# Kernel optimization log

Measured on AMD Instinct MI355X. Metric: run time of the kernel, lower is better.

The kernel has to match this reference:

```python
import jax, jax.numpy as jnp
import numpy as np
from jax import lax

EPS = 1e-5  # BatchNorm eps (torch default)


def _bn_relu_conv3x3_s2(x, bn_w, bn_b, bn_m, bn_v, w, b):
    # eval-mode BatchNorm2d -> ReLU -> conv3x3 stride 2 pad 1 (NCHW)
    inv = bn_w / jnp.sqrt(bn_v + EPS)
    y = x * inv[None, :, None, None] + (bn_b - bn_m * inv)[None, :, None, None]
    y = jax.nn.relu(y)
    y = lax.conv_general_dilated(y, w, window_strides=(2, 2),
                                 padding=((1, 1), (1, 1)),
                                 dimension_numbers=("NCHW", "OIHW", "NCHW"))
    return y + b[None, :, None, None]


def _avgpool2x2(x):
    B, C, H, W = x.shape
    return x.reshape(B, C, H // 2, 2, W // 2, 2).mean(axis=(3, 5))


def setup_inputs() -> dict:
    key = jax.random.key(0)
    ks = jax.random.split(key, 24)
    C, C3 = 128, 128 // 3
    d = {"x": jax.random.normal(ks[0], (8, C, 96, 96), jnp.float32)}
    for i, p in enumerate(["f", "g", "h"]):
        base = 1 + i * 6
        d[p + "_bn_w"] = jax.random.uniform(ks[base], (C,), jnp.float32, 0.5, 1.5)
        d[p + "_bn_b"] = jax.random.normal(ks[base + 1], (C,), jnp.float32) * 0.1
        d[p + "_bn_m"] = jax.random.normal(ks[base + 2], (C,), jnp.float32) * 0.1
        d[p + "_bn_v"] = jax.random.uniform(ks[base + 3], (C,), jnp.float32, 0.5, 1.5)
        d[p + "_w"] = jax.random.normal(ks[base + 4], (C, C, 3, 3), jnp.float32) * (1.0 / np.sqrt(9 * C))
        d[p + "_b"] = jax.random.normal(ks[base + 5], (C,), jnp.float32) * 0.01
    d["se_cw"] = jax.random.normal(ks[19], (C3, 2 * C), jnp.float32) * (1.0 / np.sqrt(2 * C))
    d["se_cb"] = jax.random.normal(ks[20], (C3,), jnp.float32) * 0.01
    d["se_uw"] = jax.random.normal(ks[21], (C, C3), jnp.float32) * (1.0 / np.sqrt(C3))
    d["se_ub"] = jax.random.normal(ks[22], (C,), jnp.float32) * 0.01
    d["gamma"] = jax.random.normal(ks[23], (1,), jnp.float32) * 0.5
    return d


def reference(x, f_bn_w, f_bn_b, f_bn_m, f_bn_v, f_w, f_b,
              g_bn_w, g_bn_b, g_bn_m, g_bn_v, g_w, g_b,
              h_bn_w, h_bn_b, h_bn_m, h_bn_v, h_w, h_b,
              se_cw, se_cb, se_uw, se_ub, gamma):
    B, C, H, W = x.shape
    left = _avgpool2x2(x)  # isPrimary=False branch -> [B,C,H/2,W/2]

    f = _bn_relu_conv3x3_s2(x, f_bn_w, f_bn_b, f_bn_m, f_bn_v, f_w, f_b)
    g = _bn_relu_conv3x3_s2(x, g_bn_w, g_bn_b, g_bn_m, g_bn_v, g_w, g_b)
    h = _bn_relu_conv3x3_s2(x, h_bn_w, h_bn_b, h_bn_m, h_bn_v, h_w, h_b)

    Ho, Wo = f.shape[2], f.shape[3]
    N = Ho * Wo
    ff = f.reshape(B, C, N)
    gg = g.reshape(B, C, N)
    hh = h.reshape(B, C, N)

    # s = softmax over last axis of f^T g : [B, N, N]
    scores = jnp.einsum("bcn,bcm->bnm", ff, gg)
    attn = jax.nn.softmax(scores, axis=2)
    s = jnp.einsum("bcn,bnm->bcm", hh, attn).reshape(B, C, Ho, Wo)
    s = gamma[0] * s

    # CompetitiveSE: global-avg x and s -> concat(2C) -> ReLU/1x1(C//3) -> ReLU/1x1(C)
    wx = x.mean(axis=(2, 3))          # [B, C]
    ws = s.mean(axis=(2, 3))          # [B, C]
    wcat = jnp.concatenate([wx, ws], axis=1)  # [B, 2C]
    se = jax.nn.relu(wcat) @ se_cw.T + se_cb
    se = jax.nn.relu(se) @ se_uw.T + se_ub    # [B, C]

    return (left + s) * (1.0 + se[:, :, None, None])
```

## Files before the change

### kernel.cpp

```cpp
#include <hip/hip_runtime.h>
#include <hip/hip_bf16.h>

#define B_   8
#define C_   128
#define H_   96
#define W_   96
#define HP_  98
#define HO_  48
#define N_   2304
#define K_CONV 1152
#define PLANE_IN  9216
#define TOT_OUT (B_*C_*N_)

typedef __attribute__((ext_vector_type(8))) short          s16x8;
typedef __attribute__((ext_vector_type(8))) unsigned short u16x8;
typedef __attribute__((ext_vector_type(4))) unsigned short u16x4;
typedef __attribute__((ext_vector_type(4))) float          f32x4;

#define SW(row, q)   (((row) << 6) + ((((q) ^ (((row) >> 1) & 3))) << 4))
#define SW8(row, q)  (((row) << 7) + ((((q) ^ ((row) & 7))) << 4))
#define SW16(row, q) (((row) << 8) + ((((q) ^ ((row) & 15))) << 4))

__device__ __forceinline__ ushort f2bf(float f) {
  __hip_bfloat16 h = __float2bfloat16(f);
  return *reinterpret_cast<ushort*>(&h);
}

__device__ __forceinline__ float block_reduce_sum_256(float v) {
  #pragma unroll
  for (int o = 32; o > 0; o >>= 1) v += __shfl_down(v, o, 64);
  __shared__ float r[4];
  int lane = threadIdx.x & 63, wv = threadIdx.x >> 6;
  if (lane == 0) r[wv] = v;
  __syncthreads();
  float s = 0.f;
  if (threadIdx.x == 0) s = r[0] + r[1] + r[2] + r[3];
  __syncthreads();
  return s;
}

__global__ void k_prep(const float* __restrict__ w0, const float* __restrict__ b0,
                       const float* __restrict__ m0, const float* __restrict__ v0,
                       const float* __restrict__ w1, const float* __restrict__ b1,
                       const float* __restrict__ m1, const float* __restrict__ v1,
                       const float* __restrict__ w2, const float* __restrict__ b2,
                       const float* __restrict__ m2, const float* __restrict__ v2,
                       float* __restrict__ inv, float* __restrict__ beta) {
  int p = blockIdx.x, c = threadIdx.x;
  const float* w = (p == 0 ? w0 : p == 1 ? w1 : w2);
  const float* bb = (p == 0 ? b0 : p == 1 ? b1 : b2);
  const float* m = (p == 0 ? m0 : p == 1 ? m1 : m2);
  const float* v = (p == 0 ? v0 : p == 1 ? v1 : v2);
  if (c < C_) {
    float iv = w[c] / sqrtf(v[c] + 1e-5f);
    inv[p * 128 + c] = iv;
    beta[p * 128 + c] = bb[c] - m[c] * iv;
  }
}

__global__ __launch_bounds__(256) void k_prep_w(const float* __restrict__ w0,
                                                const float* __restrict__ w1,
                                                const float* __restrict__ w2,
                                                ushort* __restrict__ o0,
                                                ushort* __restrict__ o1,
                                                ushort* __restrict__ o2) {
  int p = blockIdx.y;
  const float* w = (p == 0 ? w0 : p == 1 ? w1 : w2);
  ushort* wb = (p == 0 ? o0 : p == 1 ? o1 : o2);
  int id = blockIdx.x * 256 + threadIdx.x;
  if (id >= C_ * K_CONV) return;
  int co = id / K_CONV, rem = id - co * K_CONV;
  int tap = rem >> 7, ci = rem & 127;
  wb[id] = f2bf(w[co * K_CONV + ci * 9 + tap]);
}

__global__ __launch_bounds__(256) void k_prep_y(const float* __restrict__ x,
                                                const float* __restrict__ pinv,
                                                const float* __restrict__ pbeta,
                                                ushort* __restrict__ y0,
                                                ushort* __restrict__ y1,
                                                ushort* __restrict__ y2) {
  const int h1 = blockIdx.x, b = blockIdx.y, t = threadIdx.x;
  ushort* ys[3] = {y0 + (size_t)b * HP_ * HP_ * C_,
                   y1 + (size_t)b * HP_ * HP_ * C_,
                   y2 + (size_t)b * HP_ * HP_ * C_};
  u16x8 zer = (u16x8)0;
  if (h1 == 0 || h1 == HP_ - 1) {
    for (int p = 0; p < 3; ++p)
      for (int g = t; g < HP_ * C_ / 8; g += 256)
        *(u16x8*)(ys[p] + (size_t)h1 * HP_ * C_ + g * 8) = zer;
    return;
  }
  __shared__ float xs[128][97];
  const int h = h1 - 1;
  const float* xb = x + (size_t)b * C_ * PLANE_IN + h * W_;
  for (int id = t; id < 128 * 24; id += 256) {
    int ci = id / 24, w4 = id - ci * 24;
    float4 v = *(const float4*)(xb + (size_t)ci * PLANE_IN + w4 * 4);
    xs[ci][w4 * 4 + 0] = v.x; xs[ci][w4 * 4 + 1] = v.y;
    xs[ci][w4 * 4 + 2] = v.z; xs[ci][w4 * 4 + 3] = v.w;
  }
  __syncthreads();
  if (t < 32) {
    int side = t >> 4, cg = t & 15;
    for (int p = 0; p < 3; ++p)
      *(u16x8*)(ys[p] + ((size_t)h1 * HP_ + (side ? HP_ - 1 : 0)) * C_ + cg * 8) = zer;
  }
  for (int p = 0; p < 3; ++p) {
    const float* inv = pinv + p * 128;
    const float* bet = pbeta + p * 128;
    for (int g = t; g < 96 * 16; g += 256) {
      int wdx = g >> 4, cg = g & 15;
      u16x8 o;
      #pragma unroll
      for (int k = 0; k < 8; ++k) {
        int ci = cg * 8 + k;
        o[k] = f2bf(fmaxf(xs[ci][wdx] * inv[ci] + bet[ci], 0.f));
      }
      *(u16x8*)(ys[p] + ((size_t)h1 * HP_ + (wdx + 1)) * C_ + cg * 8) = o;
    }
  }
}

__global__ __launch_bounds__(256) void k_meanx(const float* __restrict__ x,
                                               float* __restrict__ wcat) {
  int bc = blockIdx.x;
  const float* p = x + (size_t)bc * PLANE_IN;
  float s = 0.f;
  for (int i = threadIdx.x; i < PLANE_IN; i += 256) s += p[i];
  s = block_reduce_sum_256(s);
  if (threadIdx.x == 0) {
    int b = bc >> 7, c = bc & 127;
    wcat[b * 256 + c] = fmaxf(s * (1.f / PLANE_IN), 0.f);
  }
}

__global__ __launch_bounds__(256) void k_conv3(
    const ushort* __restrict__ y0, const ushort* __restrict__ y1, const ushort* __restrict__ y2,
    const ushort* __restrict__ w0, const ushort* __restrict__ w1, const ushort* __restrict__ w2,
    const float* __restrict__ bi0, const float* __restrict__ bi1, const float* __restrict__ bi2,
    ushort* __restrict__ fo, ushort* __restrict__ go, ushort* __restrict__ ho) {
  __shared__ __align__(16) char smem[16384];
  char* As = smem;
  char* Bs = smem + 8192;
  const int br = blockIdx.y, b = blockIdx.z, n0 = blockIdx.x * 64;
  const int t = threadIdx.x, l = t & 63, w = t >> 6;
  const ushort* yb = (br == 0 ? y0 : br == 1 ? y1 : y2) + (size_t)b * HP_ * HP_ * C_;
  const ushort* wb = (br == 0 ? w0 : br == 1 ? w1 : w2);
  const float* bias = (br == 0 ? bi0 : br == 1 ? bi1 : bi2);
  const int pos = t >> 2, q = t & 3;
  const int n_glob = n0 + pos;
  const int oh = n_glob / HO_, ow = n_glob - oh * HO_;
  const int mh = (w & 1) * 64, nh = (w >> 1) * 32;
  f32x4 acc[4][2];
  #pragma unroll
  for (int i = 0; i < 4; ++i)
    #pragma unroll
    for (int j = 0; j < 2; ++j) acc[i][j] = (f32x4)0.f;

  for (int k0 = 0; k0 < K_CONV; k0 += 32) {
    int tap = k0 >> 7, ci0 = k0 & 127;
    int kh = tap / 3, kw = tap - kh * 3;
    #pragma unroll
    for (int g2 = 0; g2 < 2; ++g2) {
      int g = t + g2 * 256, row = g >> 2, qq = g & 3;
      u16x8 d = *(const u16x8*)(wb + row * K_CONV + k0 + qq * 8);
      *(u16x8*)(As + SW(row, qq)) = d;
    }
    {
      int h1 = 2 * oh + kh, w1 = 2 * ow + kw;
      u16x8 d = *(const u16x8*)(yb + ((size_t)h1 * HP_ + w1) * C_ + ci0 + q * 8);
      *(u16x8*)(Bs + SW(pos, q)) = d;
    }
    __syncthreads();
    s16x8 af[4], bf[2];
    #pragma unroll
    for (int i = 0; i < 4; ++i) {
      int r = mh + i * 16 + (l & 15);
      af[i] = *(const s16x8*)(As + SW(r, (l >> 4)));
    }
    #pragma unroll
    for (int j = 0; j < 2; ++j) {
      int r = nh + j * 16 + (l & 15);
      bf[j] = *(const s16x8*)(Bs + SW(r, (l >> 4)));
    }
    #pragma unroll
    for (int i = 0; i < 4; ++i)
      #pragma unroll
      for (int j = 0; j < 2; ++j)
        acc[i][j] = __builtin_amdgcn_mfma_f32_16x16x32_bf16(af[i], bf[j], acc[i][j], 0, 0, 0);
    __syncthreads();
  }

  if (br < 2) {
    ushort* out = (br == 0) ? fo : go;
    ushort* tb = (ushort*)smem;
    #pragma unroll
    for (int i = 0; i < 4; ++i) {
      int co4 = mh + i * 16 + (l >> 4) * 4;
      float4 bi = *(const float4*)&bias[co4];
      float bia[4] = {bi.x, bi.y, bi.z, bi.w};
      #pragma unroll
      for (int j = 0; j < 2; ++j) {
        int pp = nh + j * 16 + (l & 15);
        #pragma unroll
        for (int r = 0; r < 4; ++r)
          tb[pp * 128 + co4 + r] = f2bf(acc[i][j][r] + bia[r]);
      }
    }
    __syncthreads();
    #pragma unroll
    for (int it = 0; it < 4; ++it) {
      int g = t + it * 256;
      int row = g >> 4, gg = g & 15;
      u16x8 d = *(const u16x8*)(tb + row * 128 + gg * 8);
      *(u16x8*)(out + ((size_t)b * N_ + n0 + row) * C_ + gg * 8) = d;
    }
  } else {
    ushort* tb = (ushort*)smem;
    #pragma unroll
    for (int i = 0; i < 4; ++i) {
      int co4 = mh + i * 16 + (l >> 4) * 4;
      float4 bi = *(const float4*)&bias[co4];
      float bia[4] = {bi.x, bi.y, bi.z, bi.w};
      #pragma unroll
      for (int j = 0; j < 2; ++j) {
        int pp = nh + j * 16 + (l & 15);
        #pragma unroll
        for (int r = 0; r < 4; ++r)
          tb[(co4 + r) * 64 + pp] = f2bf(acc[i][j][r] + bia[r]);
      }
    }
    __syncthreads();
    for (int g = t; g < 1024; g += 256) {
      int co = g >> 3, off2 = (g & 7) * 8;
      u16x8 d = *(const u16x8*)(tb + co * 64 + off2);
      *(u16x8*)(ho + ((size_t)b * C_ + co) * N_ + n0 + off2) = d;
    }
  }
}

__global__ __launch_bounds__(256) void k_stats(const ushort* __restrict__ f,
                                               const ushort* __restrict__ g,
                                               float2* __restrict__ pstats) {
  __shared__ __align__(16) char smem[32768];
  char* fs = smem;
  char* gs = smem + 16384;
  const int b = blockIdx.z, n0 = blockIdx.x * 64, mz = blockIdx.y;
  const int t = threadIdx.x, l = t & 63, w = t >> 6, lo = l & 15, quad = l >> 4;
  const ushort* fb = f + (size_t)b * N_ * C_;
  const ushort* gb = g + (size_t)b * N_ * C_;
  #pragma unroll
  for (int it = 0; it < 4; ++it) {
    int G = t + it * 256, row = G >> 4, g16 = G & 15;
    *(u16x8*)(fs + SW16(row, g16)) = *(const u16x8*)(fb + (size_t)(n0 + row) * C_ + g16 * 8);
  }
  __syncthreads();
  s16x8 af[4];
  #pragma unroll
  for (int ks = 0; ks < 4; ++ks)
    af[ks] = *(const s16x8*)(fs + SW16(w * 16 + lo, ks * 4 + quad));
  float mloc[4], lloc[4];
  #pragma unroll
  for (int r = 0; r < 4; ++r) { mloc[r] = -1e30f; lloc[r] = 0.f; }
  const int m_beg = mz * 576;

  for (int i9 = 0; i9 < 9; ++i9) {
    int m0 = m_beg + i9 * 64;
    __syncthreads();
    #pragma unroll
    for (int it = 0; it < 4; ++it) {
      int G = t + it * 256, row = G >> 4, g16 = G & 15;
      *(u16x8*)(gs + SW16(row, g16)) = *(const u16x8*)(gb + (size_t)(m0 + row) * C_ + g16 * 8);
    }
    __syncthreads();
    f32x4 acc[4];
    #pragma unroll
    for (int j = 0; j < 4; ++j) acc[j] = (f32x4)0.f;
    #pragma unroll
    for (int ks = 0; ks < 4; ++ks)
      #pragma unroll
      for (int j = 0; j < 4; ++j) {
        s16x8 bf = *(const s16x8*)(gs + SW16(j * 16 + lo, ks * 4 + quad));
        acc[j] = __builtin_amdgcn_mfma_f32_16x16x32_bf16(af[ks], bf, acc[j], 0, 0, 0);
      }
    #pragma unroll
    for (int r = 0; r < 4; ++r) {
      float vmax = fmaxf(fmaxf(acc[0][r], acc[1][r]), fmaxf(acc[2][r], acc[3][r]));
      float mn = fmaxf(mloc[r], vmax);
      lloc[r] = lloc[r] * __expf(mloc[r] - mn) +
                __expf(acc[0][r] - mn) + __expf(acc[1][r] - mn) +
                __expf(acc[2][r] - mn) + __expf(acc[3][r] - mn);
      mloc[r] = mn;
    }
  }
  #pragma unroll
  for (int r = 0; r < 4; ++r) {
    #pragma unroll
    for (int o = 1; o < 16; o <<= 1) {
      float mo = __shfl_xor(mloc[r], o, 64);
      float lo2 = __shfl_xor(lloc[r], o, 64);
      float mn = fmaxf(mloc[r], mo);
      lloc[r] = lloc[r] * __expf(mloc[r] - mn) + lo2 * __expf(mo - mn);
      mloc[r] = mn;
    }
  }
  if (lo == 0) {
    #pragma unroll
    for (int r = 0; r < 4; ++r)
      pstats[((size_t)mz * B_ + b) * N_ + n0 + w * 16 + quad * 4 + r] =
          make_float2(mloc[r], lloc[r]);
  }
}

__global__ __launch_bounds__(256) void k_stats_red(const float2* __restrict__ p,
                                                   float2* __restrict__ stats) {
  int idx = blockIdx.x * 256 + threadIdx.x;
  if (idx >= B_ * N_) return;
  float mx = -1e30f, ls = 0.f;
  #pragma unroll
  for (int z = 0; z < 4; ++z) {
    float2 s = p[(size_t)z * B_ * N_ + idx];
    float mn = fmaxf(mx, s.x);
    ls = ls * __expf(mx - mn) + s.y * __expf(s.x - mn);
    mx = mn;
  }
  stats[idx] = make_float2(mx, ls);
}

__global__ __launch_bounds__(256) void k_attn_out(const ushort* __restrict__ f,
                                                  const ushort* __restrict__ g,
                                                  const ushort* __restrict__ h,
                                                  const float2* __restrict__ stats,
                                                  float* __restrict__ spart) {
  __shared__ __align__(16) char smem[35072];
  const int b = blockIdx.z, m0 = blockIdx.x * 64, nz = blockIdx.y;
  const int t = threadIdx.x, l = t & 63, w = t >> 6, lo = l & 15, quad = l >> 4;
  const ushort* fb = f + (size_t)b * N_ * C_;
  const ushort* gb = g + (size_t)b * N_ * C_;
  const ushort* hb = h + (size_t)b * C_ * N_;
  const float2* stb = stats + (size_t)b * N_;
  s16x8 bg[4][4];
  #pragma unroll
  for (int j = 0; j < 4; ++j)
    #pragma unroll
    for (int ks = 0; ks < 4; ++ks)
      bg[j][ks] = *(const s16x8*)(gb + (size_t)(m0 + j * 16 + lo) * C_ + (ks * 4 + quad) * 8);
  f32x4 accs[2][4];
  #pragma unroll
  for (int i = 0; i < 2; ++i)
    #pragma unroll
    for (int j = 0; j < 4; ++j) accs[i][j] = (f32x4)0.f;
  const int n_beg = nz * 576;

  for (int i9 = 0; i9 < 9; ++i9) {
    int nb = n_beg + i9 * 64;
    char* pT = smem + ((i9 & 1) << 13);
    s16x8 af[4], ah[2][2];
    #pragma unroll
    for (int ks = 0; ks < 4; ++ks)
      af[ks] = *(const s16x8*)(fb + (size_t)(nb + w * 16 + lo) * C_ + (ks * 4 + quad) * 8);
    #pragma unroll
    for (int i = 0; i < 2; ++i)
      #pragma unroll
      for (int ks = 0; ks < 2; ++ks)
        ah[i][ks] = *(const s16x8*)(hb + (size_t)((2 * w + i) * 16 + lo) * N_ + nb + (ks * 4 + quad) * 8);
    f32x4 sc[4];
    #pragma unroll
    for (int j = 0; j < 4; ++j) sc[j] = (f32x4)0.f;
    #pragma unroll
    for (int ks = 0; ks < 4; ++ks)
      #pragma unroll
      for (int j = 0; j < 4; ++j)
        sc[j] = __builtin_amdgcn_mfma_f32_16x16x32_bf16(af[ks], bg[j][ks], sc[j], 0, 0, 0);
    float mxr[4], ilr[4];
    #pragma unroll
    for (int r = 0; r < 4; ++r) {
      float2 st = stb[nb + w * 16 + quad * 4 + r];
      mxr[r] = st.x; ilr[r] = 1.f / st.y;
    }
    const int nl = w * 16 + quad * 4;
    #pragma unroll
    for (int j = 0; j < 4; ++j) {
      u16x4 pv;
      #pragma unroll
      for (int r = 0; r < 4; ++r)
        pv[r] = f2bf(__expf(sc[j][r] - mxr[r]) * ilr[r]);
      *(u16x4*)(pT + SW8(j * 16 + lo, nl >> 3) + (nl & 7) * 2) = pv;
    }
    __syncthreads();
    #pragma unroll
    for (int ks = 0; ks < 2; ++ks)
      #pragma unroll
      for (int j = 0; j < 4; ++j) {
        s16x8 bp = *(const s16x8*)(pT + SW8(j * 16 + lo, ks * 4 + quad));
        accs[0][j] = __builtin_amdgcn_mfma_f32_16x16x32_bf16(ah[0][ks], bp, accs[0][j], 0, 0, 0);
        accs[1][j] = __builtin_amdgcn_mfma_f32_16x16x32_bf16(ah[1][ks], bp, accs[1][j], 0, 0, 0);
      }
  }
  __syncthreads();
  float* ss = (float*)smem;
  #pragma unroll
  for (int i = 0; i < 2; ++i) {
    int c0 = (2 * w + i) * 16 + quad * 4;
    #pragma unroll
    for (int j = 0; j < 4; ++j) {
      int m = j * 16 + lo;
      #pragma unroll
      for (int r = 0; r < 4; ++r)
        ss[(c0 + r) * 68 + m] = accs[i][j][r];
    }
  }
  __syncthreads();
  float* outp = spart + (size_t)nz * TOT_OUT + (size_t)b * C_ * N_ + m0;
  #pragma unroll
  for (int it = 0; it < 8; ++it) {
    int idx = t + it * 256;
    int c = idx >> 4, mq = idx & 15;
    float4 v = *(const float4*)&ss[c * 68 + mq * 4];
    *(float4*)&outp[(size_t)c * N_ + mq * 4] = v;
  }
}

__global__ __launch_bounds__(256) void k_sred(const float* __restrict__ spart,
                                              const float* __restrict__ gammap,
                                              float* __restrict__ sbuf) {
  int idx = blockIdx.x * 256 + threadIdx.x;
  if (idx >= TOT_OUT) return;
  float s = spart[idx] + spart[(size_t)TOT_OUT + idx] +
            spart[2 * (size_t)TOT_OUT + idx] + spart[3 * (size_t)TOT_OUT + idx];
  sbuf[idx] = gammap[0] * s;
}

__global__ __launch_bounds__(256) void k_means(const float* __restrict__ s,
                                               float* __restrict__ wcat) {
  int bc = blockIdx.x;
  const float* p = s + (size_t)bc * N_;
  float sm = 0.f;
  for (int i = threadIdx.x; i < N_; i += 256) sm += p[i];
  sm = block_reduce_sum_256(sm);
  if (threadIdx.x == 0) {
    int b = bc >> 7, c = bc & 127;
    wcat[b * 256 + 128 + c] = fmaxf(sm * (1.f / N_), 0.f);
  }
}

__global__ __launch_bounds__(128) void k_se(const float* __restrict__ wcat,
                                            const float* __restrict__ cw,
                                            const float* __restrict__ cb,
                                            const float* __restrict__ uw,
                                            const float* __restrict__ ub,
                                            float* __restrict__ se) {
  const int b = blockIdx.x, t = threadIdx.x;
  __shared__ float wc[256];
  __shared__ float s1[42];
  wc[t] = wcat[b * 256 + t];
  wc[128 + t] = wcat[b * 256 + 128 + t];
  __syncthreads();
  if (t < 42) {
    float a = cb[t];
    const float* r = cw + (size_t)t * 256;
    for (int k = 0; k < 256; ++k) a += wc[k] * r[k];
    s1[t] = fmaxf(a, 0.f);
  }
  __syncthreads();
  {
    float a = ub[t];
    const float* r = uw + (size_t)t * 42;
    for (int j = 0; j < 42; ++j) a += s1[j] * r[j];
    se[b * 128 + t] = a;
  }
}

__global__ __launch_bounds__(256) void k_final(const float* __restrict__ x,
                                               const float* __restrict__ s,
                                               const float* __restrict__ se,
                                               float* __restrict__ out) {
  int idx = blockIdx.x * 256 + threadIdx.x;
  if (idx >= TOT_OUT) return;
  int m  = idx % N_;
  int bc = idx / N_;
  int oh = m / HO_, ow = m - oh * HO_;
  const float* xp = x + (size_t)bc * PLANE_IN;
  int ih = oh * 2, iw = ow * 2;
  float l = 0.25f * (xp[ih * W_ + iw] + xp[ih * W_ + iw + 1] +
                     xp[(ih + 1) * W_ + iw] + xp[(ih + 1) * W_ + iw + 1]);
  out[idx] = (l + s[idx]) * (1.f + se[bc]);
}

extern "C" void kernel_launch(void* const* d_in, const int* in_sizes, int n_in,
                              void* d_out, int out_size, void* d_ws, size_t ws_size,
                              hipStream_t stream) {
  (void)in_sizes; (void)n_in; (void)out_size; (void)ws_size;
  const float* x    = (const float*)d_in[0];
  const float* bnw[3] = {(const float*)d_in[1],  (const float*)d_in[7],  (const float*)d_in[13]};
  const float* bnb[3] = {(const float*)d_in[2],  (const float*)d_in[8],  (const float*)d_in[14]};
  const float* bnm[3] = {(const float*)d_in[3],  (const float*)d_in[9],  (const float*)d_in[15]};
  const float* bnv[3] = {(const float*)d_in[4],  (const float*)d_in[10], (const float*)d_in[16]};
  const float* cw_[3] = {(const float*)d_in[5],  (const float*)d_in[11], (const float*)d_in[17]};
  const float* cbb[3] = {(const float*)d_in[6],  (const float*)d_in[12], (const float*)d_in[18]};
  const float* secw = (const float*)d_in[19];
  const float* secb = (const float*)d_in[20];
  const float* seuw = (const float*)d_in[21];
  const float* seub = (const float*)d_in[22];
  const float* gamma = (const float*)d_in[23];
  float* out = (float*)d_out;

  char* ws = (char*)d_ws;
  size_t off = 0;
  auto alloc = [&](size_t bytes) -> char* {
    char* p = ws + off;
    off = (off + bytes + 255) & ~(size_t)255;
    return p;
  };
  ushort* yp[3];
  for (int p = 0; p < 3; ++p) yp[p] = (ushort*)alloc((size_t)B_ * HP_ * HP_ * C_ * 2);
  ushort* wb[3];
  for (int p = 0; p < 3; ++p) wb[p] = (ushort*)alloc((size_t)C_ * K_CONV * 2);
  ushort* fbuf = (ushort*)alloc((size_t)B_ * N_ * C_ * 2);
  ushort* gbuf = (ushort*)alloc((size_t)B_ * N_ * C_ * 2);
  ushort* hbuf = (ushort*)alloc((size_t)B_ * C_ * N_ * 2);
  float2* pstats = (float2*)alloc((size_t)4 * B_ * N_ * 8);
  float2* stats  = (float2*)alloc((size_t)B_ * N_ * 8);
  float*  spart = (float*)alloc((size_t)4 * TOT_OUT * 4);
  float*  sbuf = (float*)alloc((size_t)TOT_OUT * 4);
  float*  wcat = (float*)alloc(B_ * 256 * 4);
  float*  sebuf = (float*)alloc(B_ * 128 * 4);
  float*  pinv  = (float*)alloc(3 * 128 * 4);
  float*  pbeta = (float*)alloc(3 * 128 * 4);

  k_prep<<<3, 128, 0, stream>>>(bnw[0], bnb[0], bnm[0], bnv[0],
                                bnw[1], bnb[1], bnm[1], bnv[1],
                                bnw[2], bnb[2], bnm[2], bnv[2], pinv, pbeta);
  k_prep_w<<<dim3((C_ * K_CONV + 255) / 256, 3), 256, 0, stream>>>(
      cw_[0], cw_[1], cw_[2], wb[0], wb[1], wb[2]);
  k_prep_y<<<dim3(HP_, B_), 256, 0, stream>>>(x, pinv, pbeta, yp[0], yp[1], yp[2]);
  k_meanx<<<B_ * C_, 256, 0, stream>>>(x, wcat);

  k_conv3<<<dim3(N_ / 64, 3, B_), 256, 0, stream>>>(yp[0], yp[1], yp[2],
                                                    wb[0], wb[1], wb[2],
                                                    cbb[0], cbb[1], cbb[2],
                                                    fbuf, gbuf, hbuf);

  k_stats<<<dim3(N_ / 64, 4, B_), 256, 0, stream>>>(fbuf, gbuf, pstats);
  k_stats_red<<<(B_ * N_ + 255) / 256, 256, 0, stream>>>(pstats, stats);
  k_attn_out<<<dim3(N_ / 64, 4, B_), 256, 0, stream>>>(fbuf, gbuf, hbuf, stats, spart);
  k_sred<<<(TOT_OUT + 255) / 256, 256, 0, stream>>>(spart, gamma, sbuf);

  k_means<<<B_ * C_, 256, 0, stream>>>(sbuf, wcat);
  k_se<<<B_, 128, 0, stream>>>(wcat, secw, secb, seuw, seub, sebuf);

  k_final<<<(TOT_OUT + 255) / 256, 256, 0, stream>>>(x, sbuf, sebuf, out);
}
```

Measured before the change: 306.8 us.

## Remap attention grids batch-fastest and stage g tile in LDS

The stats and attention-output kernels now use a flattened 1D grid in which the batch index varies fastest, which interleaves batches across the XCDs and changes how blocks share caches. In k_attn_out, the 64x128 g tile is no longer held as 16 register vectors per lane; it is staged once into swizzled LDS and reread in each MFMA inner loop. This frees many VGPRs and may raise occupancy, at the cost of extra LDS reads per iteration. The P tile double buffer moves to an offset past the g tile.

After: 304.5 us. Within noise of the previous version (-0.7%).

```diff
diff --git a/kernel.cpp b/kernel.cpp
--- a/kernel.cpp
+++ b/kernel.cpp
@@ -246,7 +246,9 @@
   __shared__ __align__(16) char smem[32768];
   char* fs = smem;
   char* gs = smem + 16384;
-  const int b = blockIdx.z, n0 = blockIdx.x * 64, mz = blockIdx.y;
+  const int blk = blockIdx.x;
+  const int b = blk & 7, t2 = blk >> 3;
+  const int n0 = (t2 % 36) * 64, mz = t2 / 36;
   const int t = threadIdx.x, l = t & 63, w = t >> 6, lo = l & 15, quad = l >> 4;
   const ushort* fb = f + (size_t)b * N_ * C_;
   const ushort* gb = g + (size_t)b * N_ * C_;
@@ -334,18 +336,22 @@
                                                   const float2* __restrict__ stats,
                                                   float* __restrict__ spart) {
   __shared__ __align__(16) char smem[35072];
-  const int b = blockIdx.z, m0 = blockIdx.x * 64, nz = blockIdx.y;
+  char* gs = smem;
+  char* pTb = smem + 16384;
+  const int blk = blockIdx.x;
+  const int b = blk & 7, t2 = blk >> 3;
+  const int m0 = (t2 % 36) * 64, nz = t2 / 36;
   const int t = threadIdx.x, l = t & 63, w = t >> 6, lo = l & 15, quad = l >> 4;
   const ushort* fb = f + (size_t)b * N_ * C_;
   const ushort* gb = g + (size_t)b * N_ * C_;
   const ushort* hb = h + (size_t)b * C_ * N_;
   const float2* stb = stats + (size_t)b * N_;
-  s16x8 bg[4][4];
-  #pragma unroll
-  for (int j = 0; j < 4; ++j)
-    #pragma unroll
-    for (int ks = 0; ks < 4; ++ks)
-      bg[j][ks] = *(const s16x8*)(gb + (size_t)(m0 + j * 16 + lo) * C_ + (ks * 4 + quad) * 8);
+  #pragma unroll
+  for (int it = 0; it < 4; ++it) {
+    int G = t + it * 256, row = G >> 4, g16 = G & 15;
+    *(u16x8*)(gs + SW16(row, g16)) = *(const u16x8*)(gb + (size_t)(m0 + row) * C_ + g16 * 8);
+  }
+  __syncthreads();
   f32x4 accs[2][4];
   #pragma unroll
   for (int i = 0; i < 2; ++i)
@@ -355,7 +361,7 @@
 
   for (int i9 = 0; i9 < 9; ++i9) {
     int nb = n_beg + i9 * 64;
-    char* pT = smem + ((i9 & 1) << 13);
+    char* pT = pTb + ((i9 & 1) << 13);
     s16x8 af[4], ah[2][2];
     #pragma unroll
     for (int ks = 0; ks < 4; ++ks)
@@ -371,8 +377,10 @@
     #pragma unroll
     for (int ks = 0; ks < 4; ++ks)
       #pragma unroll
-      for (int j = 0; j < 4; ++j)
-        sc[j] = __builtin_amdgcn_mfma_f32_16x16x32_bf16(af[ks], bg[j][ks], sc[j], 0, 0, 0);
+      for (int j = 0; j < 4; ++j) {
+        s16x8 bg = *(const s16x8*)(gs + SW16(j * 16 + lo, ks * 4 + quad));
+        sc[j] = __builtin_amdgcn_mfma_f32_16x16x32_bf16(af[ks], bg, sc[j], 0, 0, 0);
+      }
     float mxr[4], ilr[4];
     #pragma unroll
     for (int r = 0; r < 4; ++r) {
@@ -542,9 +550,9 @@
                                                     cbb[0], cbb[1], cbb[2],
                                                     fbuf, gbuf, hbuf);
 
-  k_stats<<<dim3(N_ / 64, 4, B_), 256, 0, stream>>>(fbuf, gbuf, pstats);
+  k_stats<<<1152, 256, 0, stream>>>(fbuf, gbuf, pstats);
   k_stats_red<<<(B_ * N_ + 255) / 256, 256, 0, stream>>>(pstats, stats);
-  k_attn_out<<<dim3(N_ / 64, 4, B_), 256, 0, stream>>>(fbuf, gbuf, hbuf, stats, spart);
+  k_attn_out<<<1152, 256, 0, stream>>>(fbuf, gbuf, hbuf, stats, spart);
   k_sred<<<(TOT_OUT + 255) / 256, 256, 0, stream>>>(spart, gamma, sbuf);
 
   k_means<<<B_ * C_, 256, 0, stream>>>(sbuf, wcat);
```
